# Performance work log

Hardware: AMD Instinct MI355X
Metric: run time of the kernel (lower is better)

## Reference

```python
import jax, jax.numpy as jnp
import numpy as np

N = 100_000      # nodes
E = 1_600_000    # edges
INP = 32
OUT = 32
ATTN = 32        # attn_rel_emb_dim
NREL = 16
NBASE = 8


def setup_inputs() -> dict:
    key = jax.random.key(0)
    ks = jax.random.split(key, 12)
    s = 0.1
    h = jax.random.normal(ks[0], (N, INP), jnp.float32)
    src = jax.random.randint(ks[1], (E,), 0, N)
    dst = jax.random.randint(ks[2], (E,), 0, N)
    e_type = jax.random.randint(ks[3], (E,), 0, NREL)
    weight = jax.random.normal(ks[4], (NBASE, INP, OUT), jnp.float32) * s
    w_comp = jax.random.normal(ks[5], (NREL, NBASE), jnp.float32) * s
    self_loop_weight = jax.random.normal(ks[6], (INP, OUT), jnp.float32) * s
    bias = jax.random.normal(ks[7], (OUT,), jnp.float32) * s
    attn_emb = jax.random.normal(ks[8], (NREL, ATTN), jnp.float32) * s
    A_w = jax.random.normal(ks[9], (2 * INP + ATTN, ATTN), jnp.float32) * s
    A_b = jnp.zeros((ATTN,), jnp.float32)
    B_w = jax.random.normal(ks[10], (ATTN, 1), jnp.float32) * s
    B_b = jnp.zeros((1,), jnp.float32)
    return dict(h=h, weight=weight, w_comp=w_comp, self_loop_weight=self_loop_weight,
                bias=bias, attn_emb=attn_emb, A_w=A_w, A_b=A_b, B_w=B_w, B_b=B_b,
                src=src, dst=dst, e_type=e_type)


def reference(h, weight, w_comp, self_loop_weight, bias, attn_emb,
              A_w, A_b, B_w, B_b, src, dst, e_type):
    # basis-decomposed relation weights: [num_rels, inp, out]
    rel_w = jnp.einsum('rb,bio->rio', w_comp, weight)
    # in-degree based scale (torch.log(in_degrees + 1); scale /= scale.mean())
    in_deg = jax.ops.segment_sum(jnp.ones((E,), h.dtype), dst, num_segments=N)
    scale = jnp.log(in_deg + 1.0)
    scale = scale / jnp.mean(scale)
    # per-edge message: gather relation weight, bmm with source feature
    msg = jnp.einsum('ei,eio->eo', h[src], rel_w[e_type])          # [E, OUT]
    # attention MLP over [h_src, h_dst, rel_emb]
    feat = jnp.concatenate([h[src], h[dst], attn_emb[e_type]], axis=1)  # [E, 2*INP+ATTN]
    a = jax.nn.sigmoid(jax.nn.relu(feat @ A_w + A_b) @ B_w + B_b)  # [E, 1]
    # scatter-reduce attended messages into destination nodes
    agg = jax.ops.segment_sum(a * msg, dst, num_segments=N)        # [N, OUT]
    # self-loop term (curr_emb in the aggregator)
    curr = h @ self_loop_weight                                     # [N, OUT]
    denom = jnp.maximum(in_deg, 1.0)[:, None]  # nei_edge_count normalization
    out = curr + scale[:, None] * agg / denom + bias
    return jax.nn.relu(out)
```

## Files before the change

### kernel.cpp

```cpp
#include <hip/hip_runtime.h>
#include <hip/hip_fp16.h>
#include <cstdio>
#include <cstdint>

#define NREL 16
#define NBASE 8
#define NPB 512
#define NPLACE 256

typedef _Float16 half8 __attribute__((ext_vector_type(8)));
typedef float floatx4 __attribute__((ext_vector_type(4)));

template <int CTRL>
__device__ __forceinline__ float dpp_add_f(float x) {
    int xi = __builtin_bit_cast(int, x);
    int yi = __builtin_amdgcn_update_dpp(0, xi, CTRL, 0xF, 0xF, true);
    return x + __builtin_bit_cast(float, yi);
}

__global__ __launch_bounds__(256) void k_fused1(
        const float* __restrict__ h, const float* __restrict__ A_w,
        const float* __restrict__ slw,
        const int* __restrict__ dst,
        __half* __restrict__ hA1, _Float16* __restrict__ h16,
        float* __restrict__ hA2, float* __restrict__ curr,
        int* __restrict__ histT,
        int N, int E, int nb_pre) {
    __shared__ int hist[256];
    int bx = blockIdx.x;
    int t = threadIdx.x;
    if (bx < nb_pre) {
        int w = t >> 6, l = t & 63;
        int n0 = bx * 64 + w * 16;
        if (n0 >= N) return;
        int lr = l & 15, lg = l >> 4;
        int anode = n0 + lr;
        int arc = (anode < N) ? anode : N - 1;
        int ac = lg * 8;
        float4 hv0 = *(const float4*)&h[(size_t)arc * 32 + ac];
        float4 hv1 = *(const float4*)&h[(size_t)arc * 32 + ac + 4];
        half8 af;
        af[0] = (_Float16)hv0.x; af[1] = (_Float16)hv0.y;
        af[2] = (_Float16)hv0.z; af[3] = (_Float16)hv0.w;
        af[4] = (_Float16)hv1.x; af[5] = (_Float16)hv1.y;
        af[6] = (_Float16)hv1.z; af[7] = (_Float16)hv1.w;
        if (anode < N)
            *(uint4*)&h16[(size_t)anode * 32 + ac] = *(const uint4*)&af;
        #pragma unroll
        for (int g = 0; g < 6; ++g) {
            half8 bf;
            #pragma unroll
            for (int j = 0; j < 8; ++j) {
                int i = lg * 8 + j;
                int oc = g * 16 + lr;
                float v;
                if (g < 2)      v = A_w[i * 32 + oc];
                else if (g < 4) v = A_w[(32 + i) * 32 + (oc - 32)];
                else            v = slw[i * 32 + (oc - 64)];
                bf[j] = (_Float16)v;
            }
            floatx4 d = {0.f, 0.f, 0.f, 0.f};
            d = __builtin_amdgcn_mfma_f32_16x16x32_f16(af, bf, d, 0, 0, 0);
            #pragma unroll
            for (int q = 0; q < 4; ++q) {
                int node = n0 + lg * 4 + q;
                int oc = g * 16 + lr;
                if (node < N) {
                    if (g < 2)      hA1[(size_t)node * 32 + oc] = __float2half(d[q]);
                    else if (g < 4) hA2[(size_t)node * 32 + (oc - 32)] = d[q];
                    else            curr[(size_t)node * 32 + (oc - 64)] = d[q];
                }
            }
        }
    } else {
        int nsb = (N + NPB - 1) / NPB;
        hist[t] = 0;
        __syncthreads();
        int blk = bx - nb_pre;
        int bpb = (E + NPLACE - 1) / NPLACE;
        int e0 = blk * bpb;
        int e1 = e0 + bpb; if (e1 > E) e1 = E;
        for (int e = e0 + t; e < e1; e += 256)
            atomicAdd(&hist[dst[e] >> 9], 1);
        __syncthreads();
        if (t < nsb) histT[t * NPLACE + blk] = hist[t];
    }
}

__global__ __launch_bounds__(NPLACE) void k_scanH_prep(
        int* __restrict__ histT, int* __restrict__ binTot,
        const float* __restrict__ weight, const float* __restrict__ w_comp,
        const float* __restrict__ attn_emb, const float* __restrict__ A_w,
        const float* __restrict__ A_b,
        _Float16* __restrict__ relwB16, float* __restrict__ relA, int nsb) {
    __shared__ int sd[NPLACE];
    int bx = blockIdx.x, t = threadIdx.x;
    if (bx < nsb) {
        int bin = bx;
        int v = histT[bin * NPLACE + t];
        sd[t] = v;
        __syncthreads();
        for (int off = 1; off < NPLACE; off <<= 1) {
            int x = (t >= off) ? sd[t - off] : 0;
            __syncthreads();
            sd[t] += x;
            __syncthreads();
        }
        histT[bin * NPLACE + t] = sd[t] - v;
        if (t == NPLACE - 1) binTot[bin] = sd[NPLACE - 1];
    } else {
        int pidx = (bx - nsb) * 256 + t;
        int r = pidx >> 10, rem = pidx & 1023;
        int nb = rem >> 9, lj = rem & 511;
        int l = lj >> 3, j = lj & 7;
        int i = ((l >> 4) << 3) + j;
        int o = nb * 16 + (l & 15);
        float acc = 0.f;
        #pragma unroll
        for (int b = 0; b < NBASE; ++b)
            acc += w_comp[r * NBASE + b] * weight[b * 1024 + i * 32 + o];
        relwB16[pidx] = (_Float16)acc;
        if (pidx < 512) {
            int rr = pidx >> 5, oo = pidx & 31;
            float a = A_b[oo];
            #pragma unroll 8
            for (int ii = 0; ii < 32; ++ii)
                a += attn_emb[rr * 32 + ii] * A_w[(64 + ii) * 32 + oo];
            relA[pidx] = a;
        }
    }
}

__global__ __launch_bounds__(1024) void k_scanB(int* __restrict__ binTot, int nsb) {
    __shared__ int sd[1024];
    __shared__ int carry;
    int t = threadIdx.x;
    if (t == 0) carry = 0;
    __syncthreads();
    for (int base = 0; base < nsb; base += 1024) {
        int v = (base + t < nsb) ? binTot[base + t] : 0;
        sd[t] = v;
        __syncthreads();
        for (int off = 1; off < 1024; off <<= 1) {
            int x = (t >= off) ? sd[t - off] : 0;
            __syncthreads();
            sd[t] += x;
            __syncthreads();
        }
        int c = carry;
        if (base + t < nsb) binTot[base + t] = sd[t] - v + c;
        int tot = sd[1023];
        __syncthreads();
        if (t == 0) carry = c + tot;
        __syncthreads();
    }
    if (t == 0) binTot[nsb] = carry;
}

__global__ __launch_bounds__(256) void k_fused2(
        const _Float16* __restrict__ h16, const _Float16* __restrict__ relwB16,
        __half* __restrict__ hrel16,
        const int* __restrict__ src, const int* __restrict__ dst,
        const int* __restrict__ et,
        const int* __restrict__ histT, const int* __restrict__ binTot,
        int* __restrict__ tmp,
        int N, int E, int nb_hrel) {
    __shared__ __align__(16) _Float16 tile[16 * 512];
    __shared__ int cur[256];
    int bx = blockIdx.x;
    int t = threadIdx.x;
    if (bx < nb_hrel) {
        int n0 = bx * 16;
        int l = t & 63, w = t >> 6;
        int ar = n0 + (l & 15);
        if (ar >= N) ar = N - 1;
        half8 af = *(const half8*)(h16 + (size_t)ar * 32 + ((l >> 4) << 3));
        #pragma unroll
        for (int gg = 0; gg < 8; ++gg) {
            int g = w * 8 + gg;
            half8 bf = *(const half8*)(relwB16 + (size_t)g * 512 + l * 8);
            floatx4 d = {0.f, 0.f, 0.f, 0.f};
            d = __builtin_amdgcn_mfma_f32_16x16x32_f16(af, bf, d, 0, 0, 0);
            #pragma unroll
            for (int q = 0; q < 4; ++q) {
                int row = ((l >> 4) << 2) + q;
                tile[row * 512 + g * 16 + (l & 15)] = (_Float16)d[q];
            }
        }
        __syncthreads();
        #pragma unroll
        for (int p = 0; p < 4; ++p) {
            int idx = p * 256 + t;
            int row = idx >> 6, c8 = (idx & 63) << 3;
            int n = n0 + row;
            if (n < N)
                *(uint4*)&hrel16[(size_t)n * 512 + c8] = *(const uint4*)&tile[row * 512 + c8];
        }
    } else {
        int nsb = (N + NPB - 1) / NPB;
        int blk = bx - nb_hrel;
        if (t < nsb) cur[t] = histT[t * NPLACE + blk] + binTot[t];
        __syncthreads();
        int bpb = (E + NPLACE - 1) / NPLACE;
        int e0 = blk * bpb;
        int e1 = e0 + bpb; if (e1 > E) e1 = E;
        for (int e = e0 + t; e < e1; e += 256) {
            int d = dst[e];
            int pos = atomicAdd(&cur[d >> 9], 1);
            tmp[pos] = src[e] | (et[e] << 17) | ((d & 511) << 21);
        }
    }
}

__global__ __launch_bounds__(256) void k_sortbin(
        const int* __restrict__ tmp, int* __restrict__ packed,
        const int* __restrict__ binTot,
        int* __restrict__ rowptr, float* __restrict__ scale_s,
        int N, int E) {
    __shared__ int cnt[NPB];
    __shared__ int sa[256];
    __shared__ float sf[256];
    int t = threadIdx.x;
    int bin = blockIdx.x;
    int n0 = bin * NPB;
    cnt[t] = 0; cnt[t + 256] = 0;
    __syncthreads();
    int start = binTot[bin], end = binTot[bin + 1];
    for (int i = start + t; i < end; i += 256)
        atomicAdd(&cnt[(tmp[i] >> 21) & 511], 1);
    __syncthreads();
    int c0 = cnt[2 * t], c1 = cnt[2 * t + 1];
    sa[t] = c0 + c1;
    __syncthreads();
    for (int off = 1; off < 256; off <<= 1) {
        int x = (t >= off) ? sa[t - off] : 0;
        __syncthreads();
        sa[t] += x;
        __syncthreads();
    }
    int excl0 = sa[t] - (c0 + c1);
    int excl1 = excl0 + c0;
    int nA = n0 + 2 * t, nB = n0 + 2 * t + 1;
    if (nA <= N) rowptr[nA] = start + excl0;
    if (nB <= N) rowptr[nB] = start + excl1;
    float f = 0.f;
    if (nA < N) f += logf((float)c0 + 1.f);
    if (nB < N) f += logf((float)c1 + 1.f);
    sf[t] = f;
    __syncthreads();
    for (int s2 = 128; s2 > 0; s2 >>= 1) {
        if (t < s2) sf[t] += sf[t + s2];
        __syncthreads();
    }
    if (t == 0) atomicAdd(scale_s, sf[0]);
    cnt[2 * t] = start + excl0;
    cnt[2 * t + 1] = start + excl1;
    __syncthreads();
    for (int i = start + t; i < end; i += 256) {
        int rec = tmp[i];
        int dl = (rec >> 21) & 511;
        int pos = atomicAdd(&cnt[dl], 1);
        packed[pos] = rec;
    }
}

__global__ __launch_bounds__(256) void k_node_agg(
        const __half* __restrict__ hrel16, const __half* __restrict__ hA1,
        const float* __restrict__ hA2, const float* __restrict__ relA,
        const float* __restrict__ B_w, const float* __restrict__ B_b,
        const float* __restrict__ curr, const float* __restrict__ bias,
        const int* __restrict__ rowptr,
        const int* __restrict__ packed, const float* __restrict__ scale_s,
        float* __restrict__ out, int N) {
    __shared__ float relA_l[512];
    int t = threadIdx.x;
    relA_l[t] = relA[t];
    relA_l[t + 256] = relA[t + 256];
    __syncthreads();
    int wave = t >> 6, t64 = t & 63;
    int half = t64 >> 5, o = t64 & 31;
    int n = blockIdx.x * 4 + wave;
    if (n >= N) return;
    int r0 = rowptr[n], r1 = rowptr[n + 1];
    float hA2n = hA2[n * 32 + o];
    float bwo = B_w[o];
    float bb  = B_b[0];
    float acc = 0.f;
    for (int c0 = r0; c0 < r1; c0 += 64) {
        int j = c0 + t64;
        int pk = (j < r1) ? packed[j] : 0;
        int m = r1 - c0; if (m > 64) m = 64;
        for (int k = 0; k < m; k += 8) {
            int iA = k + half, iB = k + 2 + half, iC = k + 4 + half, iD = k + 6 + half;
            int pkA = __shfl(pk, iA, 64);
            int pkB = __shfl(pk, iB, 64);
            int pkC = __shfl(pk, iC, 64);
            int pkD = __shfl(pk, iD, 64);
            int sA = pkA & 0x1FFFF, rA = (pkA >> 17) & 15;
            int sB = pkB & 0x1FFFF, rB = (pkB >> 17) & 15;
            int sC = pkC & 0x1FFFF, rC = (pkC >> 17) & 15;
            int sD = pkD & 0x1FFFF, rD = (pkD >> 17) & 15;
            float msgA = __half2float(hrel16[(size_t)sA * 512 + (rA << 5) + o]);
            float msgB = __half2float(hrel16[(size_t)sB * 512 + (rB << 5) + o]);
            float msgC = __half2float(hrel16[(size_t)sC * 512 + (rC << 5) + o]);
            float msgD = __half2float(hrel16[(size_t)sD * 512 + (rD << 5) + o]);
            float a1A  = __half2float(hA1[(sA << 5) + o]);
            float a1B  = __half2float(hA1[(sB << 5) + o]);
            float a1C  = __half2float(hA1[(sC << 5) + o]);
            float a1D  = __half2float(hA1[(sD << 5) + o]);
            float zA = a1A + hA2n + relA_l[(rA << 5) + o];
            float zB = a1B + hA2n + relA_l[(rB << 5) + o];
            float zC = a1C + hA2n + relA_l[(rC << 5) + o];
            float zD = a1D + hA2n + relA_l[(rD << 5) + o];
            float pA = fmaxf(zA, 0.f) * bwo;
            float pB = fmaxf(zB, 0.f) * bwo;
            float pC = fmaxf(zC, 0.f) * bwo;
            float pD = fmaxf(zD, 0.f) * bwo;
            pA = dpp_add_f<0x111>(pA); pB = dpp_add_f<0x111>(pB);
            pC = dpp_add_f<0x111>(pC); pD = dpp_add_f<0x111>(pD);
            pA = dpp_add_f<0x112>(pA); pB = dpp_add_f<0x112>(pB);
            pC = dpp_add_f<0x112>(pC); pD = dpp_add_f<0x112>(pD);
            pA = dpp_add_f<0x114>(pA); pB = dpp_add_f<0x114>(pB);
            pC = dpp_add_f<0x114>(pC); pD = dpp_add_f<0x114>(pD);
            pA = dpp_add_f<0x118>(pA); pB = dpp_add_f<0x118>(pB);
            pC = dpp_add_f<0x118>(pC); pD = dpp_add_f<0x118>(pD);
            pA = dpp_add_f<0x142>(pA); pB = dpp_add_f<0x142>(pB);
            pC = dpp_add_f<0x142>(pC); pD = dpp_add_f<0x142>(pD);
            pA = __shfl(pA, 31, 32) + bb;
            pB = __shfl(pB, 31, 32) + bb;
            pC = __shfl(pC, 31, 32) + bb;
            pD = __shfl(pD, 31, 32) + bb;
            float aA = 1.f / (1.f + __expf(-pA));
            float aB = 1.f / (1.f + __expf(-pB));
            float aC = 1.f / (1.f + __expf(-pC));
            float aD = 1.f / (1.f + __expf(-pD));
            acc += (iA < m) ? aA * msgA : 0.f;
            acc += (iB < m) ? aB * msgB : 0.f;
            acc += (iC < m) ? aC * msgC : 0.f;
            acc += (iD < m) ? aD * msgD : 0.f;
        }
    }
    acc += __shfl_xor(acc, 32, 64);
    if (half == 0) {
        float deg = (float)(r1 - r0);
        float smean = scale_s[0] / (float)N;
        float scale = logf(deg + 1.0f);
        float v = curr[n * 32 + o] + (scale / smean) * acc / fmaxf(deg, 1.f) + bias[o];
        out[n * 32 + o] = fmaxf(v, 0.f);
    }
}

extern "C" void kernel_launch(void* const* d_in, const int* in_sizes, int n_in,
                              void* d_out, int out_size, void* d_ws, size_t ws_size,
                              hipStream_t stream) {
    const float* h        = (const float*)d_in[0];
    const float* weight   = (const float*)d_in[1];
    const float* w_comp   = (const float*)d_in[2];
    const float* slw      = (const float*)d_in[3];
    const float* bias     = (const float*)d_in[4];
    const float* attn_emb = (const float*)d_in[5];
    const float* A_w      = (const float*)d_in[6];
    const float* A_b      = (const float*)d_in[7];
    const float* B_w      = (const float*)d_in[8];
    const float* B_b      = (const float*)d_in[9];
    const int*   src      = (const int*)d_in[10];
    const int*   dst      = (const int*)d_in[11];
    const int*   et       = (const int*)d_in[12];
    float*       out      = (float*)d_out;

    int N = in_sizes[0] / 32;
    int E = in_sizes[10];
    int nsb = (N + NPB - 1) / NPB;

    char* ws = (char*)d_ws;
    size_t off = 0;
    auto alloc = [&](size_t nbytes) {
        char* p = ws + off;
        off += (nbytes + 63) & ~((size_t)63);
        return p;
    };
    float*     scale_s = (float*)    alloc(4);
    size_t zero_bytes = off;
    int*       rowptr  = (int*)      alloc((size_t)(N + 1) * 4);
    int*       histT   = (int*)      alloc((size_t)nsb * NPLACE * 4);
    int*       binTot  = (int*)      alloc((size_t)(nsb + 1) * 4);
    _Float16*  relwB16 = (_Float16*) alloc((size_t)NREL * 1024 * 2);
    float*     relA    = (float*)    alloc((size_t)NREL * 32 * 4);
    __half*    hA1     = (__half*)   alloc((size_t)N * 32 * 2);
    _Float16*  h16     = (_Float16*) alloc((size_t)N * 32 * 2);
    float*     hA2     = (float*)    alloc((size_t)N * 32 * 4);
    float*     curr    = (float*)    alloc((size_t)N * 32 * 4);
    int*       tmp     = (int*)      alloc((size_t)E * 4);
    int*       packed  = (int*)      alloc((size_t)E * 4);
    __half*    hrel16  = (__half*)   alloc((size_t)N * 512 * 2);
    size_t need = off;

    if (ws_size < need) {
        fprintf(stderr, "kernel_launch: ws too small (%zu < %zu bytes) — no work launched\n",
                ws_size, need);
        return;
    }

    (void)hipMemsetAsync(d_ws, 0, zero_bytes, stream);

    int nb_pre = (N + 63) / 64;
    k_fused1<<<nb_pre + NPLACE, 256, 0, stream>>>(
        h, A_w, slw, dst, hA1, h16, hA2, curr, histT, N, E, nb_pre);

    k_scanH_prep<<<nsb + 64, NPLACE, 0, stream>>>(
        histT, binTot, weight, w_comp, attn_emb, A_w, A_b, relwB16, relA, nsb);
    k_scanB<<<1, 1024, 0, stream>>>(binTot, nsb);

    int nb_hrel = (N + 15) / 16;
    k_fused2<<<nb_hrel + NPLACE, 256, 0, stream>>>(
        h16, relwB16, hrel16, src, dst, et, histT, binTot, tmp, N, E, nb_hrel);

    k_sortbin<<<nsb, 256, 0, stream>>>(tmp, packed, binTot, rowptr, scale_s, N, E);

    k_node_agg<<<(N + 3) / 4, 256, 0, stream>>>(
        hrel16, hA1, hA2, relA, B_w, B_b, curr, bias,
        rowptr, packed, scale_s, out, N);
}
```

Baseline: 163.1 us.

## Fold bin scan into consumers, widen sortbin block, shrink agg unroll

Removes the single-block k_scanB launch and instead recomputes the 256-entry bin-total prefix scan redundantly inside each scatter block of k_fused2 and each k_sortbin block. k_sortbin moves to 1024-thread blocks with one node per thread for the per-bin scan, and writes rowptr[N] explicitly when N divides the bin size. k_node_agg drops the shared-memory relA staging in favour of direct global reads and halves its edge unroll from four to two per step. This saves a kernel launch and serial dependency, at the cost of redundant scan work per block and less memory-level parallelism in the aggregation loop.

Result: faster. 154.6 us (-5.2%).

```diff
diff --git a/kernel.cpp b/kernel.cpp
--- a/kernel.cpp
+++ b/kernel.cpp
@@ -131,32 +131,6 @@
     }
 }
 
-__global__ __launch_bounds__(1024) void k_scanB(int* __restrict__ binTot, int nsb) {
-    __shared__ int sd[1024];
-    __shared__ int carry;
-    int t = threadIdx.x;
-    if (t == 0) carry = 0;
-    __syncthreads();
-    for (int base = 0; base < nsb; base += 1024) {
-        int v = (base + t < nsb) ? binTot[base + t] : 0;
-        sd[t] = v;
-        __syncthreads();
-        for (int off = 1; off < 1024; off <<= 1) {
-            int x = (t >= off) ? sd[t - off] : 0;
-            __syncthreads();
-            sd[t] += x;
-            __syncthreads();
-        }
-        int c = carry;
-        if (base + t < nsb) binTot[base + t] = sd[t] - v + c;
-        int tot = sd[1023];
-        __syncthreads();
-        if (t == 0) carry = c + tot;
-        __syncthreads();
-    }
-    if (t == 0) binTot[nsb] = carry;
-}
-
 __global__ __launch_bounds__(256) void k_fused2(
         const _Float16* __restrict__ h16, const _Float16* __restrict__ relwB16,
         __half* __restrict__ hrel16,
@@ -167,6 +141,7 @@
         int N, int E, int nb_hrel) {
     __shared__ __align__(16) _Float16 tile[16 * 512];
     __shared__ int cur[256];
+    __shared__ int sd[256];
     int bx = blockIdx.x;
     int t = threadIdx.x;
     if (bx < nb_hrel) {
@@ -199,7 +174,16 @@
     } else {
         int nsb = (N + NPB - 1) / NPB;
         int blk = bx - nb_hrel;
-        if (t < nsb) cur[t] = histT[t * NPLACE + blk] + binTot[t];
+        int v = (t < nsb) ? binTot[t] : 0;
+        sd[t] = v;
+        __syncthreads();
+        for (int off = 1; off < 256; off <<= 1) {
+            int x = (t >= off) ? sd[t - off] : 0;
+            __syncthreads();
+            sd[t] += x;
+            __syncthreads();
+        }
+        if (t < nsb) cur[t] = histT[t * NPLACE + blk] + sd[t] - v;
         __syncthreads();
         int bpb = (E + NPLACE - 1) / NPLACE;
         int e0 = blk * bpb;
@@ -212,54 +196,64 @@
     }
 }
 
-__global__ __launch_bounds__(256) void k_sortbin(
+__global__ __launch_bounds__(1024) void k_sortbin(
         const int* __restrict__ tmp, int* __restrict__ packed,
         const int* __restrict__ binTot,
         int* __restrict__ rowptr, float* __restrict__ scale_s,
-        int N, int E) {
+        int N, int E, int nsb) {
     __shared__ int cnt[NPB];
-    __shared__ int sa[256];
-    __shared__ float sf[256];
+    __shared__ int sd[NPB];
+    __shared__ float sf[1024];
+    __shared__ int sstart, send;
     int t = threadIdx.x;
     int bin = blockIdx.x;
     int n0 = bin * NPB;
-    cnt[t] = 0; cnt[t + 256] = 0;
-    __syncthreads();
-    int start = binTot[bin], end = binTot[bin + 1];
-    for (int i = start + t; i < end; i += 256)
+    if (t < NPB) cnt[t] = 0;
+    if (t < 256) sd[t] = (t < nsb) ? binTot[t] : 0;
+    __syncthreads();
+    for (int off = 1; off < 256; off <<= 1) {
+        int x = (t < 256 && t >= off) ? sd[t - off] : 0;
+        __syncthreads();
+        if (t < 256) sd[t] += x;
+        __syncthreads();
+    }
+    if (t == 0) {
+        send = sd[bin];
+        sstart = (bin == 0) ? 0 : sd[bin - 1];
+    }
+    __syncthreads();
+    int start = sstart, end = send;
+    for (int i = start + t; i < end; i += 1024)
         atomicAdd(&cnt[(tmp[i] >> 21) & 511], 1);
     __syncthreads();
-    int c0 = cnt[2 * t], c1 = cnt[2 * t + 1];
-    sa[t] = c0 + c1;
-    __syncthreads();
-    for (int off = 1; off < 256; off <<= 1) {
-        int x = (t >= off) ? sa[t - off] : 0;
-        __syncthreads();
-        sa[t] += x;
-        __syncthreads();
-    }
-    int excl0 = sa[t] - (c0 + c1);
-    int excl1 = excl0 + c0;
-    int nA = n0 + 2 * t, nB = n0 + 2 * t + 1;
-    if (nA <= N) rowptr[nA] = start + excl0;
-    if (nB <= N) rowptr[nB] = start + excl1;
+    if (t < NPB) sd[t] = cnt[t];
+    __syncthreads();
+    for (int off = 1; off < NPB; off <<= 1) {
+        int x = (t < NPB && t >= off) ? sd[t - off] : 0;
+        __syncthreads();
+        if (t < NPB) sd[t] += x;
+        __syncthreads();
+    }
     float f = 0.f;
-    if (nA < N) f += logf((float)c0 + 1.f);
-    if (nB < N) f += logf((float)c1 + 1.f);
+    if (t < NPB) {
+        int node = n0 + t;
+        int excl = sd[t] - cnt[t];
+        if (node <= N) rowptr[node] = start + excl;
+        if (node < N) f = logf((float)cnt[t] + 1.f);
+    }
+    if (t == 0 && bin == nsb - 1 && (N % NPB) == 0) rowptr[N] = end;
     sf[t] = f;
     __syncthreads();
-    for (int s2 = 128; s2 > 0; s2 >>= 1) {
+    for (int s2 = 512; s2 > 0; s2 >>= 1) {
         if (t < s2) sf[t] += sf[t + s2];
         __syncthreads();
     }
     if (t == 0) atomicAdd(scale_s, sf[0]);
-    cnt[2 * t] = start + excl0;
-    cnt[2 * t + 1] = start + excl1;
-    __syncthreads();
-    for (int i = start + t; i < end; i += 256) {
+    if (t < NPB) cnt[t] = start + sd[t] - cnt[t];
+    __syncthreads();
+    for (int i = start + t; i < end; i += 1024) {
         int rec = tmp[i];
-        int dl = (rec >> 21) & 511;
-        int pos = atomicAdd(&cnt[dl], 1);
+        int pos = atomicAdd(&cnt[(rec >> 21) & 511], 1);
         packed[pos] = rec;
     }
 }
@@ -272,11 +266,7 @@
         const int* __restrict__ rowptr,
         const int* __restrict__ packed, const float* __restrict__ scale_s,
         float* __restrict__ out, int N) {
-    __shared__ float relA_l[512];
     int t = threadIdx.x;
-    relA_l[t] = relA[t];
-    relA_l[t + 256] = relA[t + 256];
-    __syncthreads();
     int wave = t >> 6, t64 = t & 63;
     int half = t64 >> 5, o = t64 & 31;
     int n = blockIdx.x * 4 + wave;
@@ -290,54 +280,32 @@
         int j = c0 + t64;
         int pk = (j < r1) ? packed[j] : 0;
         int m = r1 - c0; if (m > 64) m = 64;
-        for (int k = 0; k < m; k += 8) {
-            int iA = k + half, iB = k + 2 + half, iC = k + 4 + half, iD = k + 6 + half;
-            int pkA = __shfl(pk, iA, 64);
-            int pkB = __shfl(pk, iB, 64);
-            int pkC = __shfl(pk, iC, 64);
-            int pkD = __shfl(pk, iD, 64);
+        for (int k = 0; k < m; k += 4) {
+            int idxA = k + half;
+            int idxB = k + 2 + half;
+            int pkA = __shfl(pk, idxA, 64);
+            int pkB = __shfl(pk, idxB, 64);
             int sA = pkA & 0x1FFFF, rA = (pkA >> 17) & 15;
             int sB = pkB & 0x1FFFF, rB = (pkB >> 17) & 15;
-            int sC = pkC & 0x1FFFF, rC = (pkC >> 17) & 15;
-            int sD = pkD & 0x1FFFF, rD = (pkD >> 17) & 15;
             float msgA = __half2float(hrel16[(size_t)sA * 512 + (rA << 5) + o]);
+            float a1A  = __half2float(hA1[(sA << 5) + o]);
             float msgB = __half2float(hrel16[(size_t)sB * 512 + (rB << 5) + o]);
-            float msgC = __half2float(hrel16[(size_t)sC * 512 + (rC << 5) + o]);
-            float msgD = __half2float(hrel16[(size_t)sD * 512 + (rD << 5) + o]);
-            float a1A  = __half2float(hA1[(sA << 5) + o]);
             float a1B  = __half2float(hA1[(sB << 5) + o]);
-            float a1C  = __half2float(hA1[(sC << 5) + o]);
-            float a1D  = __half2float(hA1[(sD << 5) + o]);
-            float zA = a1A + hA2n + relA_l[(rA << 5) + o];
-            float zB = a1B + hA2n + relA_l[(rB << 5) + o];
-            float zC = a1C + hA2n + relA_l[(rC << 5) + o];
-            float zD = a1D + hA2n + relA_l[(rD << 5) + o];
+            float zA = a1A + hA2n + relA[(rA << 5) + o];
+            float zB = a1B + hA2n + relA[(rB << 5) + o];
             float pA = fmaxf(zA, 0.f) * bwo;
             float pB = fmaxf(zB, 0.f) * bwo;
-            float pC = fmaxf(zC, 0.f) * bwo;
-            float pD = fmaxf(zD, 0.f) * bwo;
             pA = dpp_add_f<0x111>(pA); pB = dpp_add_f<0x111>(pB);
-            pC = dpp_add_f<0x111>(pC); pD = dpp_add_f<0x111>(pD);
             pA = dpp_add_f<0x112>(pA); pB = dpp_add_f<0x112>(pB);
-            pC = dpp_add_f<0x112>(pC); pD = dpp_add_f<0x112>(pD);
             pA = dpp_add_f<0x114>(pA); pB = dpp_add_f<0x114>(pB);
-            pC = dpp_add_f<0x114>(pC); pD = dpp_add_f<0x114>(pD);
             pA = dpp_add_f<0x118>(pA); pB = dpp_add_f<0x118>(pB);
-            pC = dpp_add_f<0x118>(pC); pD = dpp_add_f<0x118>(pD);
             pA = dpp_add_f<0x142>(pA); pB = dpp_add_f<0x142>(pB);
-            pC = dpp_add_f<0x142>(pC); pD = dpp_add_f<0x142>(pD);
             pA = __shfl(pA, 31, 32) + bb;
             pB = __shfl(pB, 31, 32) + bb;
-            pC = __shfl(pC, 31, 32) + bb;
-            pD = __shfl(pD, 31, 32) + bb;
             float aA = 1.f / (1.f + __expf(-pA));
             float aB = 1.f / (1.f + __expf(-pB));
-            float aC = 1.f / (1.f + __expf(-pC));
-            float aD = 1.f / (1.f + __expf(-pD));
-            acc += (iA < m) ? aA * msgA : 0.f;
-            acc += (iB < m) ? aB * msgB : 0.f;
-            acc += (iC < m) ? aC * msgC : 0.f;
-            acc += (iD < m) ? aD * msgD : 0.f;
+            acc += (idxA < m) ? aA * msgA : 0.f;
+            acc += (idxB < m) ? aB * msgB : 0.f;
         }
     }
     acc += __shfl_xor(acc, 32, 64);
@@ -409,13 +377,12 @@
 
     k_scanH_prep<<<nsb + 64, NPLACE, 0, stream>>>(
         histT, binTot, weight, w_comp, attn_emb, A_w, A_b, relwB16, relA, nsb);
-    k_scanB<<<1, 1024, 0, stream>>>(binTot, nsb);
 
     int nb_hrel = (N + 15) / 16;
     k_fused2<<<nb_hrel + NPLACE, 256, 0, stream>>>(
         h16, relwB16, hrel16, src, dst, et, histT, binTot, tmp, N, E, nb_hrel);
 
-    k_sortbin<<<nsb, 256, 0, stream>>>(tmp, packed, binTot, rowptr, scale_s, N, E);
+    k_sortbin<<<nsb, 1024, 0, stream>>>(tmp, packed, binTot, rowptr, scale_s, N, E, nsb);
 
     k_node_agg<<<(N + 3) / 4, 256, 0, stream>>>(
         hrel16, hA1, hA2, relA, B_w, B_b, curr, bias,
```
